# Kernel optimization log

Measured on AMD Instinct MI355X. Metric: run time of the kernel, lower is better.

## Reference

```python
import jax, jax.numpy as jnp
import numpy as np

B, L, D, N_ORIG, GD, K_TARGET = 8, 512, 1024, 8192, 64, 256
_PI, _PJ = np.triu_indices(L, k=1)  # all global pairs i<j, shared across batch


def setup_inputs() -> dict:
    key = jax.random.key(0)
    k1, k2, k3 = jax.random.split(key, 3)
    x = jax.random.normal(k1, (B, L, D), jnp.float32)
    source = jax.random.uniform(k2, (B, L, N_ORIG), jnp.float32)
    W = jax.random.normal(k3, (GD, D), jnp.float32) * 0.02  # group_proj weight (out,in), no bias
    return {"x": x, "source": source, "W": W, "target_len": K_TARGET}


def _merge_single(x, s, W, r_step, pi, pj):
    # x: (S,D), s: (S,N). One greedy global merge step (r_step = S//2 >= r_total).
    S = x.shape[0]
    g = x @ W.T                                   # (S, GD)
    gn = jnp.linalg.norm(g, axis=-1)              # token weights (g.norm)
    gu = g / jnp.maximum(gn, 1e-12)[:, None]      # F.normalize(g, dim=-1)
    sim = (gu[pi] * gu[pj]).sum(-1)               # (P,) cosine sim of each pair
    # deterministic order: (-sim, i, j); lexsort's last key is primary
    order = jnp.lexsort((pj, pi, -sim))
    si = pi[order]
    sj = pj[order]

    # sequential greedy disjoint (mutual-exclusion) selection
    def body(carry, ij):
        partner, isj, cnt = carry
        i, j = ij
        used_i = (partner[i] >= 0) | isj[i]
        used_j = (partner[j] >= 0) | isj[j]
        sel = (~used_i) & (~used_j) & (cnt < r_step)
        partner = partner.at[i].set(jnp.where(sel, j, partner[i]))
        isj = isj.at[j].set(isj[j] | sel)
        return (partner, isj, cnt + sel.astype(jnp.int32)), None

    init = (jnp.full((S,), -1, jnp.int32), jnp.zeros((S,), bool), jnp.int32(0))
    (partner, isj, _), _ = jax.lax.scan(body, init, (si, sj))

    # kept tokens (everything not a merged-away j), in original order; greedy on a
    # complete graph always selects exactly r_step pairs, so K = S - r_step is static
    K = S - r_step
    keep = jnp.argsort(isj.astype(jnp.int32), stable=True)[:K]  # (K,)
    pk = partner[keep]
    has_p = pk >= 0
    pjx = jnp.where(has_p, pk, keep)  # safe partner index
    wi = gn[keep]
    wj = gn[pjx]
    tot = wi + wj + 1e-8
    xm = jnp.where(has_p[:, None], (wi[:, None] * x[keep] + wj[:, None] * x[pjx]) / tot[:, None], x[keep])
    sm = jnp.where(has_p[:, None], s[keep] + s[pjx], s[keep])
    return xm, sm


def reference(x, source, W, target_len):
    Bb, Ll, Dd = x.shape
    r_total = Ll - target_len
    if r_total <= 0:
        return x, source
    # with target_len = L//2, r_total <= floor(L/2): single greedy step (faithful)
    r_step = min(r_total, Ll // 2)
    pi = jnp.asarray(_PI, jnp.int32)
    pj = jnp.asarray(_PJ, jnp.int32)
    f = lambda xb, sb: _merge_single(xb, sb, W, r_step, pi, pj)
    return jax.vmap(f)(x, source)
```

## Files before the change

kernel.cpp:

```cpp
#include <hip/hip_runtime.h>

#define B_ 8
#define L_ 512
#define D_ 1024
#define N_ 8192
#define GD_ 64
#define K_ 256

__global__ __launch_bounds__(128) void gproj_kernel(const float* __restrict__ x,
                                                    const float* __restrict__ W,
                                                    float* __restrict__ gu,
                                                    float* __restrict__ gn) {
  const int KC = 128;
  __shared__ __align__(16) float xs[16][KC];
  __shared__ __align__(16) float wsT[GD_][KC + 4];
  int blk = blockIdx.x;
  int b = blk >> 5;
  int t0 = (blk & 31) * 16;
  int tid = threadIdx.x;
  int dg = tid & 15, tg = tid >> 4;
  const float* xb = x + ((size_t)b * L_ + t0) * D_;
  float acc[2][4][4];
#pragma unroll
  for (int tk = 0; tk < 2; ++tk)
#pragma unroll
    for (int dd = 0; dd < 4; ++dd)
#pragma unroll
      for (int c = 0; c < 4; ++c) acc[tk][dd][c] = 0.f;
  for (int kc = 0; kc < D_; kc += KC) {
    for (int f = tid; f < 16 * KC / 4; f += 128) {
      int t = f >> 5, k4 = f & 31;
      *(float4*)&xs[t][k4 * 4] = *(const float4*)(xb + (size_t)t * D_ + kc + k4 * 4);
    }
    for (int f = tid; f < GD_ * KC / 4; f += 128) {
      int d = f >> 5, k4 = f & 31;
      *(float4*)&wsT[d][k4 * 4] = *(const float4*)(W + (size_t)d * D_ + kc + k4 * 4);
    }
    __syncthreads();
#pragma unroll 4
    for (int kk = 0; kk < KC; kk += 4) {
      float4 xv0 = *(const float4*)&xs[tg][kk];
      float4 xv1 = *(const float4*)&xs[tg + 8][kk];
#pragma unroll
      for (int dd = 0; dd < 4; ++dd) {
        float4 wv = *(const float4*)&wsT[dg * 4 + dd][kk];
        acc[0][dd][0] += xv0.x * wv.x;
        acc[0][dd][1] += xv0.y * wv.y;
        acc[0][dd][2] += xv0.z * wv.z;
        acc[0][dd][3] += xv0.w * wv.w;
        acc[1][dd][0] += xv1.x * wv.x;
        acc[1][dd][1] += xv1.y * wv.y;
        acc[1][dd][2] += xv1.z * wv.z;
        acc[1][dd][3] += xv1.w * wv.w;
      }
    }
    __syncthreads();
  }
#pragma unroll
  for (int tk = 0; tk < 2; ++tk) {
    float g[4];
    double ss = 0.0;
#pragma unroll
    for (int dd = 0; dd < 4; ++dd) {
      g[dd] = (acc[tk][dd][0] + acc[tk][dd][1]) + (acc[tk][dd][2] + acc[tk][dd][3]);
      ss += (double)g[dd] * (double)g[dd];
    }
#pragma unroll
    for (int off = 1; off < 16; off <<= 1) ss += __shfl_xor(ss, off);
    float gnv = (float)sqrt(ss);
    float dn = fmaxf(gnv, 1e-12f);
    int t = t0 + tg + tk * 8;
    if (dg == 0) gn[(size_t)b * L_ + t] = gnv;
    float* gup = gu + ((size_t)b * L_ + t) * GD_ + dg * 4;
#pragma unroll
    for (int dd = 0; dd < 4; ++dd) gup[dd] = g[dd] / dn;
  }
}

__global__ __launch_bounds__(256) void sim_kernel(const float* __restrict__ gu,
                                                  float* __restrict__ simo) {
  __shared__ __align__(16) float BsT[GD_][36];
  int b = blockIdx.z;
  int i0 = blockIdx.y * 32, j0 = blockIdx.x * 32;
  const float* gb = gu + (size_t)b * L_ * GD_;
  int tid = threadIdx.x;
  for (int f = tid; f < 32 * GD_; f += 256) {
    int r = f >> 6, k = f & 63;
    BsT[k][r] = gb[(size_t)(j0 + r) * GD_ + k];
  }
  int r = tid >> 3, c4 = (tid & 7) * 4;
  float af[GD_];
  const float4* arow = (const float4*)(gb + (size_t)(i0 + r) * GD_);
#pragma unroll
  for (int q = 0; q < 16; ++q) *(float4*)&af[q * 4] = arow[q];
  __syncthreads();
  double a0 = 0, a1 = 0, a2 = 0, a3 = 0;
#pragma unroll
  for (int k = 0; k < GD_; ++k) {
    double a = (double)af[k];
    float4 bv = *(const float4*)&BsT[k][c4];
    a0 += a * (double)bv.x;
    a1 += a * (double)bv.y;
    a2 += a * (double)bv.z;
    a3 += a * (double)bv.w;
  }
  float4 o;
  o.x = (float)a0; o.y = (float)a1; o.z = (float)a2; o.w = (float)a3;
  *(float4*)(simo + (size_t)b * L_ * L_ + (size_t)(i0 + r) * L_ + (j0 + c4)) = o;
}

__global__ __launch_bounds__(256) void topk_kernel(const float* __restrict__ sim,
                                                   unsigned long long* __restrict__ cand) {
  int wid = blockIdx.x * 4 + (threadIdx.x >> 6);
  int b = wid >> 9;
  int a = wid & 511;
  int lane = threadIdx.x & 63;
  const float* row = sim + ((size_t)b * L_ + a) * L_;
  int c0 = lane * 8;
  float4 v0 = *(const float4*)(row + c0);
  float4 v1 = *(const float4*)(row + c0 + 4);
  float vv[8] = {v0.x, v0.y, v0.z, v0.w, v1.x, v1.y, v1.z, v1.w};
  unsigned long long k[8];
#pragma unroll
  for (int s = 0; s < 8; ++s) {
    int bb = c0 + s;
    if (bb == a) {
      k[s] = 0;
    } else {
      unsigned u = __float_as_uint(vv[s]);
      u = (u & 0x80000000u) ? ~u : (u | 0x80000000u);
      int i = a < bb ? a : bb, j = a < bb ? bb : a;
      k[s] = ((unsigned long long)u << 18) |
             (unsigned long long)(0x3FFFFu - (((unsigned)i << 9) | (unsigned)j));
    }
  }
  unsigned long long* out = cand + ((size_t)b * L_ + a) * 16;
#pragma unroll
  for (int pass = 0; pass < 16; ++pass) {
    unsigned long long m = k[0];
#pragma unroll
    for (int s = 1; s < 8; ++s) m = k[s] > m ? k[s] : m;
#pragma unroll
    for (int off = 32; off; off >>= 1) {
      unsigned long long o = __shfl_xor(m, off);
      if (o > m) m = o;
    }
#pragma unroll
    for (int s = 0; s < 8; ++s)
      if (k[s] == m) k[s] = 0;
    if (lane == 0) out[pass] = m;
  }
}

__global__ __launch_bounds__(512) void match_kernel(const float* __restrict__ sim,
                                                    const unsigned long long* __restrict__ cand,
                                                    int* __restrict__ keepI,
                                                    int* __restrict__ keepJ) {
  int b = blockIdx.x;
  const float* S = sim + (size_t)b * L_ * L_;
  const unsigned long long* C = cand + (size_t)b * L_ * 16;
  __shared__ unsigned long long candL[L_][16];
  __shared__ unsigned long long bestkey[L_];
  __shared__ short partner[L_];
  __shared__ short liveA[L_], liveB[L_], rescanQ[L_];
  __shared__ unsigned char liveF[L_], needs[L_], head[L_];
  __shared__ int nLiveNew, nQ;
  int tid = threadIdx.x;
  int wave = tid >> 6, lane = tid & 63;
  for (int f = tid; f < L_ * 8; f += 512)
    ((ulonglong2*)candL)[f] = ((const ulonglong2*)C)[f];
  if (tid < L_) {
    partner[tid] = -1;
    liveF[tid] = 1;
    needs[tid] = 1;
    head[tid] = 0;
    liveA[tid] = (short)tid;
    bestkey[tid] = 0ull;
  }
  if (tid == 0) {
    nLiveNew = L_;
    nQ = 0;
  }
  __syncthreads();
  for (int round = 0; round < 300; ++round) {
    int nLive = nLiveNew;
    if (nLive == 0) break;
    short* cur = (round & 1) ? liveB : liveA;
    short* nxt = (round & 1) ? liveA : liveB;
    for (int idx = tid; idx < nLive; idx += 512) {
      int a = cur[idx];
      if (needs[a]) {
        int h = head[a];
        unsigned long long bk = 0ull;
        while (h < 16) {
          unsigned long long key = candL[a][h];
          if (key) {
            unsigned pk = 0x3FFFFu - (unsigned)(key & 0x3FFFFull);
            int i = (int)(pk >> 9), j = (int)(pk & 511u);
            int p = (i == a) ? j : i;
            if (liveF[p]) { bk = key; break; }
          }
          ++h;
        }
        head[a] = (unsigned char)h;
        if (bk) {
          bestkey[a] = bk;
          needs[a] = 0;
        } else {
          int q = atomicAdd(&nQ, 1);
          rescanQ[q] = (short)a;
        }
      }
    }
    __syncthreads();
    int nq = nQ;
    for (int q = wave; q < nq; q += 8) {
      int a = rescanQ[q];
      unsigned long long mk = 0ull;
      for (int kk = lane; kk < nLive; kk += 64) {
        int bb = cur[kk];
        if (bb != a) {
          float sv = S[(size_t)a * L_ + bb];
          unsigned u = __float_as_uint(sv);
          u = (u & 0x80000000u) ? ~u : (u | 0x80000000u);
          int i = a < bb ? a : bb, j = a < bb ? bb : a;
          unsigned long long key =
              ((unsigned long long)u << 18) |
              (unsigned long long)(0x3FFFFu - (((unsigned)i << 9) | (unsigned)j));
          if (key > mk) mk = key;
        }
      }
#pragma unroll
      for (int off = 32; off; off >>= 1) {
        unsigned long long o = __shfl_xor(mk, off);
        if (o > mk) mk = o;
      }
      if (lane == 0) {
        bestkey[a] = mk;
        needs[a] = 0;
      }
    }
    if (tid == 0) nLiveNew = 0;
    __syncthreads();
    for (int idx = tid; idx < nLive; idx += 512) {
      int a = cur[idx];
      unsigned pk = 0x3FFFFu - (unsigned)(bestkey[a] & 0x3FFFFull);
      int i = (int)(pk >> 9), j = (int)(pk & 511u);
      int p = (i == a) ? j : i;
      unsigned pk2 = 0x3FFFFu - (unsigned)(bestkey[p] & 0x3FFFFull);
      int i2 = (int)(pk2 >> 9), j2 = (int)(pk2 & 511u);
      int p2 = (i2 == p) ? j2 : i2;
      if (p2 == a) {
        partner[a] = (short)p;
        liveF[a] = 0;
      }
    }
    __syncthreads();
    for (int idx = tid; idx < nLive; idx += 512) {
      int a = cur[idx];
      if (liveF[a]) {
        unsigned pk = 0x3FFFFu - (unsigned)(bestkey[a] & 0x3FFFFull);
        int i = (int)(pk >> 9), j = (int)(pk & 511u);
        int p = (i == a) ? j : i;
        if (!liveF[p]) needs[a] = 1;
        int pos = atomicAdd(&nLiveNew, 1);
        nxt[pos] = (short)a;
      }
    }
    if (tid == 0) nQ = 0;
    __syncthreads();
  }
  if (wave == 0) {
    int base = 0;
    for (int c = 0; c < 8; ++c) {
      int a = c * 64 + lane;
      bool kept = partner[a] > a;
      unsigned long long m = __ballot(kept);
      int pos = base + (int)__popcll(m & ((1ull << lane) - 1ull));
      if (kept) {
        keepI[b * K_ + pos] = a;
        keepJ[b * K_ + pos] = partner[a];
      }
      base += (int)__popcll(m);
    }
  }
}

__global__ __launch_bounds__(256) void merge_kernel(const float* __restrict__ x,
                                                    const float* __restrict__ s,
                                                    const float* __restrict__ gn,
                                                    const int* __restrict__ keepI,
                                                    const int* __restrict__ keepJ,
                                                    float* __restrict__ xm,
                                                    float* __restrict__ sm) {
  int row = blockIdx.x;
  int b = row >> 8;
  int i = keepI[row], j = keepJ[row];
  float wi = gn[(size_t)b * L_ + i], wj = gn[(size_t)b * L_ + j];
  float tot = wi + wj + 1e-8f;
  int t = threadIdx.x;
  {
    const float4* xi = (const float4*)(x + ((size_t)b * L_ + i) * D_);
    const float4* xj = (const float4*)(x + ((size_t)b * L_ + j) * D_);
    float4* o = (float4*)(xm + (size_t)row * D_);
    float4 a = xi[t], c = xj[t];
    float4 r;
    r.x = (wi * a.x + wj * c.x) / tot;
    r.y = (wi * a.y + wj * c.y) / tot;
    r.z = (wi * a.z + wj * c.z) / tot;
    r.w = (wi * a.w + wj * c.w) / tot;
    o[t] = r;
  }
  {
    const float4* si = (const float4*)(s + ((size_t)b * L_ + i) * N_);
    const float4* sj = (const float4*)(s + ((size_t)b * L_ + j) * N_);
    float4* o = (float4*)(sm + (size_t)row * N_);
    for (int tt = t; tt < N_ / 4; tt += 256) {
      float4 a = si[tt], c = sj[tt];
      float4 r;
      r.x = a.x + c.x;
      r.y = a.y + c.y;
      r.z = a.z + c.z;
      r.w = a.w + c.w;
      o[tt] = r;
    }
  }
}

extern "C" void kernel_launch(void* const* d_in, const int* in_sizes, int n_in,
                              void* d_out, int out_size, void* d_ws, size_t ws_size,
                              hipStream_t stream) {
  (void)in_sizes; (void)n_in; (void)out_size; (void)ws_size;
  const float* x = (const float*)d_in[0];
  const float* src = (const float*)d_in[1];
  const float* W = (const float*)d_in[2];

  float* ws = (float*)d_ws;
  float* gu = ws;
  float* gn = gu + (size_t)B_ * L_ * GD_;
  float* sim = gn + (size_t)B_ * L_;
  int* keepI = (int*)(sim + (size_t)B_ * L_ * L_);
  int* keepJ = keepI + B_ * K_;
  unsigned long long* cand = (unsigned long long*)(keepJ + B_ * K_);

  float* xm = (float*)d_out;
  float* sm = xm + (size_t)B_ * K_ * D_;

  gproj_kernel<<<256, 128, 0, stream>>>(x, W, gu, gn);
  sim_kernel<<<dim3(16, 16, 8), 256, 0, stream>>>(gu, sim);
  topk_kernel<<<1024, 256, 0, stream>>>(sim, cand);
  match_kernel<<<B_, 512, 0, stream>>>(sim, cand, keepI, keepJ);
  merge_kernel<<<B_ * K_, 256, 0, stream>>>(x, src, gn, keepI, keepJ, xm, sm);
}
```

Before: 383.3 us.

## Restructure group projection as split-K with transposed W and swizzled LDS tile

A small kernel now transposes W into a (D, GD) layout. The projection kernel loads the block's whole 16-token x tile into swizzled shared memory and splits the D reduction across 16 thread groups, each holding W in registers and computing all 16 tokens. Partial sums are then reduced through shared memory. The aim is to cut the repeated W staging and syncs per K-chunk and to raise per-thread reuse, at the cost of an extra launch, about 128KB of LDS (low occupancy), and heavy register use.

Result: faster. 311.5 us (-18.7%).

```diff
diff --git a/kernel.cpp b/kernel.cpp
--- a/kernel.cpp
+++ b/kernel.cpp
@@ -7,74 +7,94 @@
 #define GD_ 64
 #define K_ 256
 
-__global__ __launch_bounds__(128) void gproj_kernel(const float* __restrict__ x,
-                                                    const float* __restrict__ W,
+#define XQ(q) ((q) ^ (((q) >> 4) & 7))
+
+__global__ __launch_bounds__(256) void wt_kernel(const float* __restrict__ W,
+                                                 float* __restrict__ Wt) {
+  int idx = blockIdx.x * 256 + threadIdx.x;
+  int d = idx >> 6, g = idx & 63;
+  Wt[idx] = W[(size_t)g * D_ + d];
+}
+
+__global__ __launch_bounds__(256) void gproj_kernel(const float* __restrict__ x,
+                                                    const float* __restrict__ Wt,
                                                     float* __restrict__ gu,
                                                     float* __restrict__ gn) {
-  const int KC = 128;
-  __shared__ __align__(16) float xs[16][KC];
-  __shared__ __align__(16) float wsT[GD_][KC + 4];
+  __shared__ __align__(16) float xs[16 * 1024];
+  __shared__ __align__(16) float red[16][16][64];
   int blk = blockIdx.x;
   int b = blk >> 5;
   int t0 = (blk & 31) * 16;
   int tid = threadIdx.x;
-  int dg = tid & 15, tg = tid >> 4;
   const float* xb = x + ((size_t)b * L_ + t0) * D_;
-  float acc[2][4][4];
-#pragma unroll
-  for (int tk = 0; tk < 2; ++tk)
-#pragma unroll
-    for (int dd = 0; dd < 4; ++dd)
-#pragma unroll
-      for (int c = 0; c < 4; ++c) acc[tk][dd][c] = 0.f;
-  for (int kc = 0; kc < D_; kc += KC) {
-    for (int f = tid; f < 16 * KC / 4; f += 128) {
-      int t = f >> 5, k4 = f & 31;
-      *(float4*)&xs[t][k4 * 4] = *(const float4*)(xb + (size_t)t * D_ + kc + k4 * 4);
-    }
-    for (int f = tid; f < GD_ * KC / 4; f += 128) {
-      int d = f >> 5, k4 = f & 31;
-      *(float4*)&wsT[d][k4 * 4] = *(const float4*)(W + (size_t)d * D_ + kc + k4 * 4);
-    }
-    __syncthreads();
-#pragma unroll 4
-    for (int kk = 0; kk < KC; kk += 4) {
-      float4 xv0 = *(const float4*)&xs[tg][kk];
-      float4 xv1 = *(const float4*)&xs[tg + 8][kk];
-#pragma unroll
-      for (int dd = 0; dd < 4; ++dd) {
-        float4 wv = *(const float4*)&wsT[dg * 4 + dd][kk];
-        acc[0][dd][0] += xv0.x * wv.x;
-        acc[0][dd][1] += xv0.y * wv.y;
-        acc[0][dd][2] += xv0.z * wv.z;
-        acc[0][dd][3] += xv0.w * wv.w;
-        acc[1][dd][0] += xv1.x * wv.x;
-        acc[1][dd][1] += xv1.y * wv.y;
-        acc[1][dd][2] += xv1.z * wv.z;
-        acc[1][dd][3] += xv1.w * wv.w;
-      }
-    }
-    __syncthreads();
-  }
-#pragma unroll
-  for (int tk = 0; tk < 2; ++tk) {
-    float g[4];
-    double ss = 0.0;
-#pragma unroll
-    for (int dd = 0; dd < 4; ++dd) {
-      g[dd] = (acc[tk][dd][0] + acc[tk][dd][1]) + (acc[tk][dd][2] + acc[tk][dd][3]);
-      ss += (double)g[dd] * (double)g[dd];
-    }
-#pragma unroll
-    for (int off = 1; off < 16; off <<= 1) ss += __shfl_xor(ss, off);
-    float gnv = (float)sqrt(ss);
-    float dn = fmaxf(gnv, 1e-12f);
-    int t = t0 + tg + tk * 8;
-    if (dg == 0) gn[(size_t)b * L_ + t] = gnv;
-    float* gup = gu + ((size_t)b * L_ + t) * GD_ + dg * 4;
-#pragma unroll
-    for (int dd = 0; dd < 4; ++dd) gup[dd] = g[dd] / dn;
-  }
+  for (int r = 0; r < 16; ++r) {
+    int idx = r * 256 + tid;
+    int tok = idx >> 8, q = idx & 255;
+    float4 v = *(const float4*)(xb + (size_t)tok * D_ + q * 4);
+    *(float4*)&xs[tok * 1024 + XQ(q) * 4] = v;
+  }
+  __syncthreads();
+  int dq = tid & 15, kg = tid >> 4;
+  float acc[16][4];
+#pragma unroll
+  for (int t = 0; t < 16; ++t)
+#pragma unroll
+    for (int d = 0; d < 4; ++d) acc[t][d] = 0.f;
+  const float* wbase = Wt + (size_t)(kg * 64) * GD_ + dq * 4;
+#pragma unroll 1
+  for (int sub = 0; sub < 4; ++sub) {
+    float4 wv[16];
+#pragma unroll
+    for (int kk = 0; kk < 16; ++kk)
+      wv[kk] = *(const float4*)(wbase + (size_t)(sub * 16 + kk) * GD_);
+#pragma unroll
+    for (int tok = 0; tok < 16; ++tok) {
+      float4 xv[4];
+#pragma unroll
+      for (int kq = 0; kq < 4; ++kq) {
+        int q = kg * 16 + sub * 4 + kq;
+        xv[kq] = *(const float4*)&xs[tok * 1024 + XQ(q) * 4];
+      }
+#pragma unroll
+      for (int kq = 0; kq < 4; ++kq) {
+        float xc[4] = {xv[kq].x, xv[kq].y, xv[kq].z, xv[kq].w};
+#pragma unroll
+        for (int c = 0; c < 4; ++c) {
+          float4 w = wv[kq * 4 + c];
+          acc[tok][0] += xc[c] * w.x;
+          acc[tok][1] += xc[c] * w.y;
+          acc[tok][2] += xc[c] * w.z;
+          acc[tok][3] += xc[c] * w.w;
+        }
+      }
+    }
+  }
+#pragma unroll
+  for (int tok = 0; tok < 16; ++tok) {
+    float4 p;
+    p.x = acc[tok][0]; p.y = acc[tok][1]; p.z = acc[tok][2]; p.w = acc[tok][3];
+    *(float4*)&red[kg][tok][dq * 4] = p;
+  }
+  __syncthreads();
+  int tok = tid >> 4, dqo = tid & 15;
+  float g[4] = {0.f, 0.f, 0.f, 0.f};
+#pragma unroll
+  for (int k = 0; k < 16; ++k) {
+    float4 p = *(const float4*)&red[k][tok][dqo * 4];
+    g[0] += p.x; g[1] += p.y; g[2] += p.z; g[3] += p.w;
+  }
+  double ss = 0.0;
+#pragma unroll
+  for (int d = 0; d < 4; ++d) ss += (double)g[d] * (double)g[d];
+#pragma unroll
+  for (int off = 1; off < 16; off <<= 1) ss += __shfl_xor(ss, off);
+  float gnv = (float)sqrt(ss);
+  float dn = fmaxf(gnv, 1e-12f);
+  int t = t0 + tok;
+  if (dqo == 0) gn[(size_t)b * L_ + t] = gnv;
+  float4 o;
+  o.x = g[0] / dn; o.y = g[1] / dn; o.z = g[2] / dn; o.w = g[3] / dn;
+  *(float4*)(gu + ((size_t)b * L_ + t) * GD_ + dqo * 4) = o;
 }
 
 __global__ __launch_bounds__(256) void sim_kernel(const float* __restrict__ gu,
@@ -336,7 +356,8 @@
   const float* W = (const float*)d_in[2];
 
   float* ws = (float*)d_ws;
-  float* gu = ws;
+  float* Wt = ws;
+  float* gu = Wt + 65536;
   float* gn = gu + (size_t)B_ * L_ * GD_;
   float* sim = gn + (size_t)B_ * L_;
   int* keepI = (int*)(sim + (size_t)B_ * L_ * L_);
@@ -346,7 +367,8 @@
   float* xm = (float*)d_out;
   float* sm = xm + (size_t)B_ * K_ * D_;
 
-  gproj_kernel<<<256, 128, 0, stream>>>(x, W, gu, gn);
+  wt_kernel<<<256, 256, 0, stream>>>(W, Wt);
+  gproj_kernel<<<256, 256, 0, stream>>>(x, Wt, gu, gn);
   sim_kernel<<<dim3(16, 16, 8), 256, 0, stream>>>(gu, sim);
   topk_kernel<<<1024, 256, 0, stream>>>(sim, cand);
   match_kernel<<<B_, 512, 0, stream>>>(sim, cand, keepI, keepJ);
```
